# Kernel tuning notes

Hardware: AMD Instinct MI355X
Metric: run time of the kernel (lower is better)

Reference implementation:

```python
import jax, jax.numpy as jnp
import numpy as np
from jax import lax

C = 256          # fpn_feats_dim
NC = 20          # num_classes
GROUPS = 16      # GroupNorm groups
EPS = 1e-5       # GroupNorm eps (torch default)
BATCH = 8
LEVELS = [(100, 128), (50, 64), (25, 32)]  # FPN level H,W for 800x1024 image, strides 8/16/32
PRIOR_BIAS = -float(np.log((1 - 0.01) / 0.01))  # ~-4.5951, FCOS prior init


def _conv3(x, w, b):
    # 3x3 stride-1 pad-1 conv, NCHW / OIHW
    y = lax.conv_general_dilated(x, w, (1, 1), 'SAME',
                                 dimension_numbers=('NCHW', 'OIHW', 'NCHW'))
    return y + b[None, :, None, None]


def _gn(x, g, b):
    n, c, h, w = x.shape
    xr = x.reshape(n, GROUPS, c // GROUPS, h, w)
    m = xr.mean(axis=(2, 3, 4), keepdims=True)
    v = xr.var(axis=(2, 3, 4), keepdims=True)
    xr = (xr - m) * lax.rsqrt(v + EPS)
    x = xr.reshape(n, c, h, w)
    return x * g[None, :, None, None] + b[None, :, None, None]


def _forward(feat0, feat1, feat2,
             cls_conv_w, cls_conv_b, cls_gn_g, cls_gn_b, cls_out_w, cls_out_b,
             reg_conv_w, reg_conv_b, reg_gn_g, reg_gn_b,
             reg_out_w, reg_out_b, ctr_w, ctr_b):
    feats = [feat0, feat1, feat2]
    all_cls, all_reg, all_ctr = [], [], []
    for f in feats:
        n = f.shape[0]
        x = f
        for i in range(2):
            x = jax.nn.relu(_gn(_conv3(x, cls_conv_w[i], cls_conv_b[i]),
                                cls_gn_g[i], cls_gn_b[i]))
        logits = _conv3(x, cls_out_w, cls_out_b)           # [N, NC, H, W]
        # view(N,-1,NC,H,W).permute(0,3,4,1,2).reshape(N,-1,NC) == NHWC flatten
        all_cls.append(logits.transpose(0, 2, 3, 1).reshape(n, -1, NC))
        t = f
        for i in range(2):
            t = jax.nn.relu(_gn(_conv3(t, reg_conv_w[i], reg_conv_b[i]),
                                reg_gn_g[i], reg_gn_b[i]))
        # bbox_reg = Sequential(conv, ReLU), then an extra relu in forward (idempotent)
        bbox = jax.nn.relu(jax.nn.relu(_conv3(t, reg_out_w, reg_out_b)))  # [N,4,H,W]
        all_reg.append(bbox.transpose(0, 2, 3, 1).reshape(n, -1, 1))      # [N,H*W*4,1]
        ctr = _conv3(t, ctr_w, ctr_b)                                     # [N,1,H,W]
        all_ctr.append(ctr.transpose(0, 2, 3, 1).reshape(n, -1, 1))       # [N,H*W,1]
    cls_cat = jnp.concatenate(all_cls, axis=1)
    reg_cat = jnp.concatenate(all_reg, axis=1)
    ctr_cat = jnp.concatenate(all_ctr, axis=1)
    return cls_cat, reg_cat, ctr_cat


def setup_inputs() -> dict:
    key = jax.random.key(0)
    ks = jax.random.split(key, 20)
    std = 0.01
    d = {}
    for i, (h, w) in enumerate(LEVELS):
        d[f"feat{i}"] = jax.random.normal(ks[i], (BATCH, C, h, w), jnp.float32)
    # classification head params
    d["cls_conv_w"] = jax.random.normal(ks[3], (2, C, C, 3, 3), jnp.float32) * std
    d["cls_conv_b"] = jnp.zeros((2, C), jnp.float32)
    d["cls_gn_g"] = jnp.ones((2, C), jnp.float32)
    d["cls_gn_b"] = jnp.zeros((2, C), jnp.float32)
    d["cls_out_w"] = jax.random.normal(ks[4], (NC, C, 3, 3), jnp.float32) * std
    d["cls_out_b"] = jnp.full((NC,), PRIOR_BIAS, jnp.float32)
    d["reg_conv_w"] = jax.random.normal(ks[5], (2, C, C, 3, 3), jnp.float32) * std
    d["reg_conv_b"] = jnp.zeros((2, C), jnp.float32)
    d["reg_gn_g"] = jnp.ones((2, C), jnp.float32)
    d["reg_gn_b"] = jnp.zeros((2, C), jnp.float32)
    d["reg_out_w"] = jax.random.normal(ks[6], (4, C, 3, 3), jnp.float32) * std
    d["reg_out_b"] = jnp.zeros((4,), jnp.float32)
    d["ctr_w"] = jax.random.normal(ks[7], (1, C, 3, 3), jnp.float32) * std
    d["ctr_b"] = jnp.zeros((1,), jnp.float32)
    return d


def reference(feat0, feat1, feat2,
              cls_conv_w, cls_conv_b, cls_gn_g, cls_gn_b, cls_out_w, cls_out_b,
              reg_conv_w, reg_conv_b, reg_gn_g, reg_gn_b,
              reg_out_w, reg_out_b, ctr_w, ctr_b):
    return _forward(feat0, feat1, feat2,
                    cls_conv_w, cls_conv_b, cls_gn_g, cls_gn_b, cls_out_w, cls_out_b,
                    reg_conv_w, reg_conv_b, reg_gn_g, reg_gn_b,
                    reg_out_w, reg_out_b, ctr_w, ctr_b)
```

## Files before the change

kernel.cpp:

```cpp
#include <hip/hip_runtime.h>

typedef unsigned short u16;
typedef __attribute__((ext_vector_type(8))) unsigned short ushort8v;
typedef __attribute__((ext_vector_type(8))) short short8v;
typedef __attribute__((ext_vector_type(4))) float floatx4;

__device__ __forceinline__ float bf2f(u16 u) {
    unsigned v = ((unsigned)u) << 16;
    float f;
    __builtin_memcpy(&f, &v, 4);
    return f;
}
__device__ __forceinline__ u16 f2bf(float f) {
    unsigned v;
    __builtin_memcpy(&v, &f, 4);
    unsigned r = (v + 0x7fffu + ((v >> 16) & 1u)) >> 16;
    return (u16)r;
}
__device__ __forceinline__ float ld(const void* p, long i, int isf) {
    return isf ? ((const float*)p)[i] : bf2f(((const u16*)p)[i]);
}
__device__ __forceinline__ void gll16(const void* g, void* l) {
    __builtin_amdgcn_global_load_lds(
        (const __attribute__((address_space(1))) unsigned int*)g,
        (__attribute__((address_space(3))) unsigned int*)l, 16, 0, 0);
}

__global__ void detect_dtype(const u16* __restrict__ gng, int* __restrict__ flag) {
    if (threadIdx.x == 0) flag[0] = (gng[0] == 0x3F80u) ? 0 : 1;
}

__global__ void conv_params(const void* ccb, const void* cgg, const void* cgb,
                            const void* rcb, const void* rgg, const void* rgb,
                            const void* cob, const void* rob, const void* ctb,
                            const int* __restrict__ flag, u16* __restrict__ dst) {
    const int isf = flag[0];
    for (int i = threadIdx.x; i < 3104; i += 256) {
        const void* src; int off;
        if (i < 512)       { src = ccb; off = i; }
        else if (i < 1024) { src = cgg; off = i - 512; }
        else if (i < 1536) { src = cgb; off = i - 1024; }
        else if (i < 2048) { src = rcb; off = i - 1536; }
        else if (i < 2560) { src = rgg; off = i - 2048; }
        else if (i < 3072) { src = rgb; off = i - 2560; }
        else if (i < 3092) { src = cob; off = i - 3072; }
        else if (i < 3096) { src = rob; off = i - 3092; }
        else if (i < 3097) { src = ctb; off = 0; }
        else               { dst[i] = 0; continue; }
        dst[i] = f2bf(ld(src, off, isf));
    }
}

__global__ void prep_w(const void* __restrict__ src, long srcOff,
                       const int* __restrict__ flag, u16* __restrict__ dst,
                       int CoutSrc, int BNr) {
    const int isf = flag[0];
    unsigned e = blockIdx.x * 256 + threadIdx.x;
    unsigned c = e & 31u;
    unsigned r = (e >> 5) % (unsigned)BNr;
    unsigned kc = (e / (32u * BNr)) % 72u;
    unsigned nt = e / (32u * BNr * 72u);
    unsigned co = nt * BNr + r;
    unsigned tap = kc >> 3, ci = (kc & 7u) * 32u + c;
    u16 v = 0;
    if (co < (unsigned)CoutSrc)
        v = f2bf(ld(src, srcOff + (long)(co * 256u + ci) * 9 + tap, isf));
    dst[e] = v;
}

__global__ void prep_w_regctr(const void* __restrict__ wreg, const void* __restrict__ wctr,
                              const int* __restrict__ flag, u16* __restrict__ dst) {
    const int isf = flag[0];
    unsigned e = blockIdx.x * 256 + threadIdx.x;
    unsigned c = e & 31u;
    unsigned r = (e >> 5) & 31u;
    unsigned kc = e / 1024u;
    unsigned tap = kc >> 3, ci = (kc & 7u) * 32u + c;
    u16 v = 0;
    if (r < 4u)       v = f2bf(ld(wreg, (long)(r * 256u + ci) * 9 + tap, isf));
    else if (r == 4u) v = f2bf(ld(wctr, (long)ci * 9 + tap, isf));
    dst[e] = v;
}

__global__ void zero_border(u16* __restrict__ buf, int H, int Wp, int Hp, int NB) {
    const int nb = 2 * Wp + 2 * H;
    unsigned idx = blockIdx.x * 256 + threadIdx.x;
    unsigned ch = idx & 31u;
    unsigned rem = idx >> 5;
    unsigned n = rem / (unsigned)nb;
    unsigned b = rem - n * nb;
    if (n >= (unsigned)NB) return;
    int ppos;
    if ((int)b < Wp) ppos = (int)b;
    else if ((int)b < 2 * Wp) ppos = (Hp - 1) * Wp + ((int)b - Wp);
    else {
        int r = (int)b - 2 * Wp;
        ppos = (1 + (r >> 1)) * Wp + ((r & 1) ? (Wp - 1) : 0);
    }
    ushort8v z = {};
    *(ushort8v*)(buf + ((long)n * (Hp * Wp) + ppos) * 256 + ch * 8) = z;
}

__global__ void nchw_to_nhwc_pad(const void* __restrict__ src, long srcOff,
                                 const int* __restrict__ flag, u16* __restrict__ dst,
                                 int S, int W, int Wp, int HpWp) {
    const int isf = flag[0];
    __shared__ u16 t[64][34];
    const int tid = threadIdx.x;
    const int n = blockIdx.z, ct = blockIdx.y;
    const int s0 = blockIdx.x * 32;
    const long base = srcOff + ((long)(n * 256 + ct * 64)) * S + s0;
#pragma unroll
    for (int i = 0; i < 8; ++i) {
        int c = i * 8 + (tid >> 5);
        t[c][tid & 31] = f2bf(ld(src, base + (long)c * S + (tid & 31), isf));
    }
    __syncthreads();
#pragma unroll
    for (int i = 0; i < 8; ++i) {
        int px = i * 4 + (tid >> 6);
        int s = s0 + px;
        int y = s / W, x = s - y * W;
        dst[((long)n * HpWp + (long)(y + 1) * Wp + (x + 1)) * 256 + ct * 64 + (tid & 63)] =
            t[tid & 63][px];
    }
}

__global__ void gn_stats(const u16* __restrict__ x, float* __restrict__ stats, int S) {
    const int n = blockIdx.x >> 4, g = blockIdx.x & 15;
    const int tid = threadIdx.x;
    float sum = 0.f, sq = 0.f;
    const u16* base = x + (long)n * S * 256 + g * 16 + (tid & 7) * 2;
    for (int p = tid >> 3; p < S; p += 32) {
        unsigned v = *(const unsigned*)(base + (long)p * 256);
        float x0 = bf2f((u16)(v & 0xffffu));
        float x1 = bf2f((u16)(v >> 16));
        sum += x0 + x1;
        sq += x0 * x0 + x1 * x1;
    }
#pragma unroll
    for (int off = 32; off > 0; off >>= 1) {
        sum += __shfl_down(sum, off, 64);
        sq  += __shfl_down(sq, off, 64);
    }
    __shared__ float red[8];
    const int wave = tid >> 6, lane = tid & 63;
    if (lane == 0) { red[wave * 2] = sum; red[wave * 2 + 1] = sq; }
    __syncthreads();
    if (tid == 0) {
        stats[(n * 16 + g) * 2]     = red[0] + red[2] + red[4] + red[6];
        stats[(n * 16 + g) * 2 + 1] = red[1] + red[3] + red[5] + red[7];
    }
}

__global__ void gn_norm_relu(const u16* __restrict__ x, const float* __restrict__ stats,
                             const u16* __restrict__ gam, const u16* __restrict__ bet,
                             u16* __restrict__ outp, int S, int W, int Wp, int HpWp,
                             float invC) {
    unsigned idx = blockIdx.x * 256 + threadIdx.x;
    unsigned c8 = idx & 31u;
    unsigned rem = idx >> 5;
    unsigned p = rem % (unsigned)S;
    unsigned n = rem / (unsigned)S;
    unsigned c0 = c8 * 8u;
    unsigned g = c0 >> 4;
    float sum = stats[(n * 16 + g) * 2], sq = stats[(n * 16 + g) * 2 + 1];
    float mean = sum * invC;
    float var = fmaxf(sq * invC - mean * mean, 0.f);
    float rstd = rsqrtf(var + 1e-5f);
    ushort8v v = *(const ushort8v*)(x + ((long)(n * S + p)) * 256 + c0);
    unsigned y = p / (unsigned)W, xc = p - y * W;
    u16* dst = outp + ((long)n * HpWp + (long)(y + 1) * Wp + (xc + 1)) * 256 + c0;
    ushort8v o;
#pragma unroll
    for (int j = 0; j < 8; ++j) {
        float xv = bf2f(v[j]);
        float r = (xv - mean) * rstd * bf2f(gam[c0 + j]) + bf2f(bet[c0 + j]);
        o[j] = f2bf(fmaxf(r, 0.f));
    }
    *(ushort8v*)dst = o;
}

template <int BN, int MODE>
__global__ __launch_bounds__(256, 2)
void conv_gemm(const u16* __restrict__ Ap, const u16* __restrict__ Wb,
               const u16* __restrict__ bias, const u16* __restrict__ bias2,
               void* __restrict__ outp, long ob1, long ob2,
               const int* __restrict__ dflag,
               int M, int n0, int S, int W, int Wp, int HpWp, int prefS) {
    static_assert(BN == 256 || BN == 32, "");
    constexpr int MI = (BN == 256) ? 4 : 2;
    constexpr int NI = (BN == 256) ? 8 : 2;
    constexpr int ASZ = 128 * 32;
    constexpr int BSZ = BN * 32;
    __shared__ __align__(16) u16 ldsA[3 * ASZ];
    __shared__ __align__(16) u16 ldsB[3 * BSZ];
    const int tid = threadIdx.x;
    const int lane = tid & 63, wave = tid >> 6;

    const unsigned NTg = gridDim.y;
    const unsigned nwg = gridDim.x * NTg;
    const unsigned lin = blockIdx.y * gridDim.x + blockIdx.x;
    const unsigned qq = nwg >> 3, rr = nwg & 7u;
    const unsigned xcd = lin & 7u, pos = lin >> 3;
    const unsigned wg =
        (xcd < rr ? xcd * (qq + 1u) : rr * (qq + 1u) + (xcd - rr) * qq) + pos;
    const int nt = (int)(wg % NTg);
    const int m0 = (int)(wg / NTg) * 128;

    int isf = 0;
    if (MODE != 0) isf = dflag[0];

    const int csw = ((lane & 3) ^ ((lane >> 2) & 3)) * 16;

    const int r0 = 32 * wave + (lane >> 2);
    int mA0 = m0 + r0;        if (mA0 > M - 1) mA0 = M - 1;
    int mA1 = m0 + r0 + 16;   if (mA1 > M - 1) mA1 = M - 1;
    const char* aL0;
    const char* aL1;
    {
        int n8 = mA0 / S, s = mA0 - n8 * S, y = s / W, x = s - y * W;
        aL0 = (const char*)(Ap + ((long)n8 * HpWp + (long)(y + 1) * Wp + (x + 1)) * 256)
              + csw;
        n8 = mA1 / S; s = mA1 - n8 * S; y = s / W; x = s - y * W;
        aL1 = (const char*)(Ap + ((long)n8 * HpWp + (long)(y + 1) * Wp + (x + 1)) * 256)
              + csw;
    }
    u16* lA0 = ldsA + (32 * wave) * 32;
    u16* lA1 = ldsA + (32 * wave + 16) * 32;

    const u16* b_tile = Wb + (long)nt * 72 * BN * 32;
    const char* bsrc0;
    u16* lB0;
    if (BN == 256) {
        bsrc0 = (const char*)b_tile + (64 * wave + (lane >> 2)) * 64 + csw;
        lB0 = ldsB + (64 * wave) * 32;
    } else {
        bsrc0 = (const char*)b_tile + (16 * wave + (lane >> 2)) * 64 + csw;
        lB0 = ldsB + wave * 16 * 32;
    }

    auto STAGE = [&](int kc, int p) {
        const int tap = kc >> 3;
        const int ty = tap / 3;
        const int tx = tap - ty * 3;
        const long aoffB = (long)((ty - 1) * Wp + (tx - 1)) * 512 + (kc & 7) * 64;
        gll16(aL0 + aoffB, lA0 + p * ASZ);
        gll16(aL1 + aoffB, lA1 + p * ASZ);
        if (BN == 256) {
            const char* bs = bsrc0 + (long)kc * 16384;
            u16* lb = lB0 + p * BSZ;
            gll16(bs,        lb);
            gll16(bs + 1024, lb + 16 * 32);
            gll16(bs + 2048, lb + 32 * 32);
            gll16(bs + 3072, lb + 48 * 32);
        } else {
            if (wave < 2) gll16(bsrc0 + (long)kc * 2048, lB0 + p * BSZ);
        }
    };

    floatx4 acc[MI][NI] = {};

    const int wm = (BN == 256) ? (wave & 1) * 64 : wave * 32;
    const int wn = (BN == 256) ? (wave >> 1) * 128 : 0;
    const int fr = lane & 15, q = lane >> 4;
    const int qs = (q ^ (fr & 3)) * 8;
    const u16* fA = ldsA + (wm + fr) * 32 + qs;
    const u16* fB = ldsB + (wn + fr) * 32 + qs;

    STAGE(0, 0);
    STAGE(1, 1);
    STAGE(2, 2);

    int p = 0;
#pragma unroll 1
    for (int kc = 0; kc < 70; ++kc) {
        if constexpr (BN == 256)
            asm volatile("s_waitcnt vmcnt(12)" ::: "memory");
        else
            asm volatile("s_waitcnt vmcnt(4)" ::: "memory");
        __builtin_amdgcn_s_barrier();
        short8v af[MI], bf[NI];
        const u16* fAp = fA + p * ASZ;
        const u16* fBp = fB + p * BSZ;
#pragma unroll
        for (int i = 0; i < MI; ++i) af[i] = *(const short8v*)(fAp + i * 16 * 32);
#pragma unroll
        for (int j = 0; j < NI; ++j) bf[j] = *(const short8v*)(fBp + j * 16 * 32);
        asm volatile("s_waitcnt lgkmcnt(0)" ::: "memory");
        __builtin_amdgcn_s_barrier();
        if (kc < 69) STAGE(kc + 3, p);
#pragma unroll
        for (int i = 0; i < MI; ++i)
#pragma unroll
            for (int j = 0; j < NI; ++j)
                acc[i][j] = __builtin_amdgcn_mfma_f32_16x16x32_bf16(af[i], bf[j],
                                                                    acc[i][j], 0, 0, 0);
        p = (p == 2) ? 0 : p + 1;
    }
    {
        if constexpr (BN == 256)
            asm volatile("s_waitcnt vmcnt(6)" ::: "memory");
        else
            asm volatile("s_waitcnt vmcnt(2)" ::: "memory");
        __builtin_amdgcn_s_barrier();
        short8v af[MI], bf[NI];
        const u16* fAp = fA + 1 * ASZ;
        const u16* fBp = fB + 1 * BSZ;
#pragma unroll
        for (int i = 0; i < MI; ++i) af[i] = *(const short8v*)(fAp + i * 16 * 32);
#pragma unroll
        for (int j = 0; j < NI; ++j) bf[j] = *(const short8v*)(fBp + j * 16 * 32);
#pragma unroll
        for (int i = 0; i < MI; ++i)
#pragma unroll
            for (int j = 0; j < NI; ++j)
                acc[i][j] = __builtin_amdgcn_mfma_f32_16x16x32_bf16(af[i], bf[j],
                                                                    acc[i][j], 0, 0, 0);
    }
    {
        asm volatile("s_waitcnt vmcnt(0)" ::: "memory");
        __builtin_amdgcn_s_barrier();
        short8v af[MI], bf[NI];
        const u16* fAp = fA + 2 * ASZ;
        const u16* fBp = fB + 2 * BSZ;
#pragma unroll
        for (int i = 0; i < MI; ++i) af[i] = *(const short8v*)(fAp + i * 16 * 32);
#pragma unroll
        for (int j = 0; j < NI; ++j) bf[j] = *(const short8v*)(fBp + j * 16 * 32);
#pragma unroll
        for (int i = 0; i < MI; ++i)
#pragma unroll
            for (int j = 0; j < NI; ++j)
                acc[i][j] = __builtin_amdgcn_mfma_f32_16x16x32_bf16(af[i], bf[j],
                                                                    acc[i][j], 0, 0, 0);
    }

    if (MODE == 0) {
        u16* out = (u16*)outp;
#pragma unroll
        for (int j = 0; j < NI; ++j) {
            const int co = nt * BN + wn + j * 16 + fr;
            const float bv = bf2f(bias[co]);
#pragma unroll
            for (int i = 0; i < MI; ++i) {
#pragma unroll
                for (int r = 0; r < 4; ++r) {
                    const int mg = m0 + wm + i * 16 + q * 4 + r;
                    if (mg < M)
                        out[(long)mg * 256 + co] = f2bf(acc[i][j][r] + bv);
                }
            }
        }
    } else {
#pragma unroll
        for (int i = 0; i < MI; ++i) {
#pragma unroll
            for (int r = 0; r < 4; ++r) {
                const int mg = m0 + wm + i * 16 + q * 4 + r;
                if (mg >= M) continue;
                const int n8 = mg / S;
                const int s = mg - n8 * S;
                const long gi = n0 + n8;
#pragma unroll
                for (int j = 0; j < NI; ++j) {
                    const int co = wn + j * 16 + fr;
                    const float v = acc[i][j][r];
                    long oi = -1;
                    float val = 0.f;
                    if (MODE == 1) {
                        if (co < 20) {
                            oi = ob1 + gi * 336000 + (long)(prefS + s) * 20 + co;
                            val = v + bf2f(bias[co]);
                        }
                    } else {
                        if (co < 4) {
                            oi = ob1 + gi * 67200 + (long)(prefS + s) * 4 + co;
                            val = fmaxf(v + bf2f(bias[co]), 0.f);
                        } else if (co == 4) {
                            oi = ob2 + gi * 16800 + (prefS + s);
                            val = v + bf2f(bias2[0]);
                        }
                    }
                    if (oi >= 0) {
                        if (isf) ((float*)outp)[oi] = val;
                        else     ((u16*)outp)[oi] = f2bf(val);
                    }
                }
            }
        }
    }
}

extern "C" void kernel_launch(void* const* d_in, const int* in_sizes, int n_in,
                              void* d_out, int out_size, void* d_ws, size_t ws_size,
                              hipStream_t stream) {
    (void)in_sizes; (void)n_in; (void)out_size;
    const void* feat[3]   = {d_in[0], d_in[1], d_in[2]};
    const void* cls_conv_w = d_in[3];
    const void* cls_conv_b = d_in[4];
    const void* cls_gn_g   = d_in[5];
    const void* cls_gn_b   = d_in[6];
    const void* cls_out_w  = d_in[7];
    const void* cls_out_b  = d_in[8];
    const void* reg_conv_w = d_in[9];
    const void* reg_conv_b = d_in[10];
    const void* reg_gn_g   = d_in[11];
    const void* reg_gn_b   = d_in[12];
    const void* reg_out_w  = d_in[13];
    const void* reg_out_b  = d_in[14];
    const void* ctr_w      = d_in[15];
    const void* ctr_b      = d_in[16];

    char* ws = (char*)d_ws;
    int*  flag     = (int*)ws;
    u16*  params   = (u16*)(ws + 1024);
    u16*  Wb       = (u16*)(ws + 8192);
    float* stats   = (float*)(ws + 5021696);
    const size_t base = 5022720;
    const size_t per_img = 6789120ull + 6553600ull + 6789120ull;
    int NB = 8;
    while (NB > 1 && base + (size_t)NB * per_img > ws_size) NB >>= 1;
    u16* feat_pad  = (u16*)(ws + base);
    u16* conv_out  = (u16*)(ws + base + (size_t)NB * 6789120ull);
    u16* norm_pad  = (u16*)(ws + base + (size_t)NB * (6789120ull + 6553600ull));

    detect_dtype<<<1, 64, 0, stream>>>((const u16*)cls_gn_g, flag);
    conv_params<<<1, 256, 0, stream>>>(cls_conv_b, cls_gn_g, cls_gn_b,
                                       reg_conv_b, reg_gn_g, reg_gn_b,
                                       cls_out_b, reg_out_b, ctr_b, flag, params);
    prep_w<<<2304, 256, 0, stream>>>(cls_conv_w, 0,      flag, Wb + 0,       256, 256);
    prep_w<<<2304, 256, 0, stream>>>(cls_conv_w, 589824, flag, Wb + 589824,  256, 256);
    prep_w<<<2304, 256, 0, stream>>>(reg_conv_w, 0,      flag, Wb + 1179648, 256, 256);
    prep_w<<<2304, 256, 0, stream>>>(reg_conv_w, 589824, flag, Wb + 1769472, 256, 256);
    prep_w<<<288,  256, 0, stream>>>(cls_out_w,  0,      flag, Wb + 2359296, 20, 32);
    prep_w_regctr<<<288, 256, 0, stream>>>(reg_out_w, ctr_w, flag, Wb + 2433024);

    const int Hs[3] = {100, 50, 25}, Wss[3] = {128, 64, 32};
    const int prefSs[3] = {0, 12800, 16000};

    for (int l = 0; l < 3; ++l) {
        const int H = Hs[l], W = Wss[l], S = H * W;
        const int Hp = H + 2, Wp = W + 2, HpWp = Hp * Wp;
        const int prefS = prefSs[l];
        const int nb = 2 * Wp + 2 * H;
        const float invC = 1.0f / (16.0f * (float)S);

        for (int n0 = 0; n0 < 8; n0 += NB) {
            const int M = NB * S;
            const int mtiles = (M + 127) / 128;
            const int zb_blocks = (NB * nb * 32 + 255) / 256;

            zero_border<<<zb_blocks, 256, 0, stream>>>(feat_pad, H, Wp, Hp, NB);
            zero_border<<<zb_blocks, 256, 0, stream>>>(norm_pad, H, Wp, Hp, NB);
            nchw_to_nhwc_pad<<<dim3(S / 32, 4, NB), 256, 0, stream>>>(
                feat[l], (long)n0 * 256 * S, flag, feat_pad, S, W, Wp, HpWp);

            conv_gemm<256, 0><<<dim3(mtiles, 1), 256, 0, stream>>>(
                feat_pad, Wb + 0, params + 0, nullptr, conv_out, 0, 0, flag,
                M, n0, S, W, Wp, HpWp, 0);
            gn_stats<<<NB * 16, 256, 0, stream>>>(conv_out, stats, S);
            gn_norm_relu<<<M / 8, 256, 0, stream>>>(conv_out, stats, params + 512,
                                                    params + 1024, norm_pad,
                                                    S, W, Wp, HpWp, invC);
            conv_gemm<256, 0><<<dim3(mtiles, 1), 256, 0, stream>>>(
                norm_pad, Wb + 589824, params + 256, nullptr, conv_out, 0, 0, flag,
                M, n0, S, W, Wp, HpWp, 0);
            gn_stats<<<NB * 16, 256, 0, stream>>>(conv_out, stats, S);
            gn_norm_relu<<<M / 8, 256, 0, stream>>>(conv_out, stats, params + 512 + 256,
                                                    params + 1024 + 256, norm_pad,
                                                    S, W, Wp, HpWp, invC);
            conv_gemm<32, 1><<<dim3(mtiles, 1), 256, 0, stream>>>(
                norm_pad, Wb + 2359296, params + 3072, nullptr, d_out, 0, 0, flag,
                M, n0, S, W, Wp, HpWp, prefS);

            conv_gemm<256, 0><<<dim3(mtiles, 1), 256, 0, stream>>>(
                feat_pad, Wb + 1179648, params + 1536, nullptr, conv_out, 0, 0, flag,
                M, n0, S, W, Wp, HpWp, 0);
            gn_stats<<<NB * 16, 256, 0, stream>>>(conv_out, stats, S);
            gn_norm_relu<<<M / 8, 256, 0, stream>>>(conv_out, stats, params + 2048,
                                                    params + 2560, norm_pad,
                                                    S, W, Wp, HpWp, invC);
            conv_gemm<256, 0><<<dim3(mtiles, 1), 256, 0, stream>>>(
                norm_pad, Wb + 1769472, params + 1536 + 256, nullptr, conv_out, 0, 0, flag,
                M, n0, S, W, Wp, HpWp, 0);
            gn_stats<<<NB * 16, 256, 0, stream>>>(conv_out, stats, S);
            gn_norm_relu<<<M / 8, 256, 0, stream>>>(conv_out, stats, params + 2048 + 256,
                                                    params + 2560 + 256, norm_pad,
                                                    S, W, Wp, HpWp, invC);
            conv_gemm<32, 2><<<dim3(mtiles, 1), 256, 0, stream>>>(
                norm_pad, Wb + 2433024, params + 3092, params + 3096,
                d_out, 2688000, 3225600, flag,
                M, n0, S, W, Wp, HpWp, prefS);
        }
    }
}
```

Before: 2.315 ms.

## Restructure triple-buffered GEMM loop to one barrier per step with MFMA priority

The K loop of the conv GEMM is reorganised. It now keeps two stages in flight and issues the next prefetch into the buffer freed in the previous iteration, so each step needs one barrier instead of two. Per-wave vmcnt waits now match the number of loads each wave issued. MFMA blocks are wrapped in s_setprio so compute waves get scheduling priority. The cost is a shorter prefetch distance, which could expose global-load latency, and the wait counts must stay exactly right for the result to be correct.

```diff
diff --git a/kernel.cpp b/kernel.cpp
--- a/kernel.cpp
+++ b/kernel.cpp
@@ -268,18 +268,7 @@
     const u16* fA = ldsA + (wm + fr) * 32 + qs;
     const u16* fB = ldsB + (wn + fr) * 32 + qs;
 
-    STAGE(0, 0);
-    STAGE(1, 1);
-    STAGE(2, 2);
-
-    int p = 0;
-#pragma unroll 1
-    for (int kc = 0; kc < 70; ++kc) {
-        if constexpr (BN == 256)
-            asm volatile("s_waitcnt vmcnt(12)" ::: "memory");
-        else
-            asm volatile("s_waitcnt vmcnt(4)" ::: "memory");
-        __builtin_amdgcn_s_barrier();
+    auto COMPUTE = [&](int p) {
         short8v af[MI], bf[NI];
         const u16* fAp = fA + p * ASZ;
         const u16* fBp = fB + p * BSZ;
@@ -287,53 +276,49 @@
         for (int i = 0; i < MI; ++i) af[i] = *(const short8v*)(fAp + i * 16 * 32);
 #pragma unroll
         for (int j = 0; j < NI; ++j) bf[j] = *(const short8v*)(fBp + j * 16 * 32);
-        asm volatile("s_waitcnt lgkmcnt(0)" ::: "memory");
-        __builtin_amdgcn_s_barrier();
-        if (kc < 69) STAGE(kc + 3, p);
+        __builtin_amdgcn_s_setprio(1);
 #pragma unroll
         for (int i = 0; i < MI; ++i)
 #pragma unroll
             for (int j = 0; j < NI; ++j)
                 acc[i][j] = __builtin_amdgcn_mfma_f32_16x16x32_bf16(af[i], bf[j],
                                                                     acc[i][j], 0, 0, 0);
+        __builtin_amdgcn_s_setprio(0);
+    };
+
+    STAGE(0, 0);
+    STAGE(1, 1);
+
+    int p = 0;
+    int pn = 2;
+#pragma unroll 1
+    for (int kc = 0; kc < 70; ++kc) {
+        if constexpr (BN == 256) {
+            asm volatile("s_waitcnt vmcnt(6)" ::: "memory");
+        } else {
+            if (wave < 2) asm volatile("s_waitcnt vmcnt(3)" ::: "memory");
+            else          asm volatile("s_waitcnt vmcnt(2)" ::: "memory");
+        }
+        __builtin_amdgcn_s_barrier();
+        STAGE(kc + 2, pn);
+        COMPUTE(p);
+        pn = p;
         p = (p == 2) ? 0 : p + 1;
     }
     {
-        if constexpr (BN == 256)
+        if constexpr (BN == 256) {
             asm volatile("s_waitcnt vmcnt(6)" ::: "memory");
-        else
-            asm volatile("s_waitcnt vmcnt(2)" ::: "memory");
+        } else {
+            if (wave < 2) asm volatile("s_waitcnt vmcnt(3)" ::: "memory");
+            else          asm volatile("s_waitcnt vmcnt(2)" ::: "memory");
+        }
         __builtin_amdgcn_s_barrier();
-        short8v af[MI], bf[NI];
-        const u16* fAp = fA + 1 * ASZ;
-        const u16* fBp = fB + 1 * BSZ;
-#pragma unroll
-        for (int i = 0; i < MI; ++i) af[i] = *(const short8v*)(fAp + i * 16 * 32);
-#pragma unroll
-        for (int j = 0; j < NI; ++j) bf[j] = *(const short8v*)(fBp + j * 16 * 32);
-#pragma unroll
-        for (int i = 0; i < MI; ++i)
-#pragma unroll
-            for (int j = 0; j < NI; ++j)
-                acc[i][j] = __builtin_amdgcn_mfma_f32_16x16x32_bf16(af[i], bf[j],
-                                                                    acc[i][j], 0, 0, 0);
+        COMPUTE(1);
     }
     {
         asm volatile("s_waitcnt vmcnt(0)" ::: "memory");
         __builtin_amdgcn_s_barrier();
-        short8v af[MI], bf[NI];
-        const u16* fAp = fA + 2 * ASZ;
-        const u16* fBp = fB + 2 * BSZ;
-#pragma unroll
-        for (int i = 0; i < MI; ++i) af[i] = *(const short8v*)(fAp + i * 16 * 32);
-#pragma unroll
-        for (int j = 0; j < NI; ++j) bf[j] = *(const short8v*)(fBp + j * 16 * 32);
-#pragma unroll
-        for (int i = 0; i < MI; ++i)
-#pragma unroll
-            for (int j = 0; j < NI; ++j)
-                acc[i][j] = __builtin_amdgcn_mfma_f32_16x16x32_bf16(af[i], bf[j],
-                                                                    acc[i][j], 0, 0, 0);
+        COMPUTE(2);
     }
 
     if (MODE == 0) {
```

New measurement: 2.600 ms. +12.3%, slower.

## Load B weight fragments directly from global into registers, bypassing LDS

Applied to the files above, without the earlier changes.

For the BN=256 conv GEMM path, weight (B) fragments are now loaded straight from global memory into registers with inline global_load_dwordx4, double-buffered across two register sets, instead of being staged through LDS. Only the A (activation) tile still goes through LDS with a 3-slot ring, and prefetch distance drops from 3 to 2. This cuts LDS traffic and LDS footprint, which may allow higher occupancy. In exchange it uses more VGPRs for the two B buffers and relies on hand-set vmcnt counts and L2 hits for the weight reads.

```diff
diff --git a/kernel.cpp b/kernel.cpp
--- a/kernel.cpp
+++ b/kernel.cpp
@@ -192,9 +192,9 @@
     constexpr int MI = (BN == 256) ? 4 : 2;
     constexpr int NI = (BN == 256) ? 8 : 2;
     constexpr int ASZ = 128 * 32;
-    constexpr int BSZ = BN * 32;
+    constexpr int BSZ = 32 * 32;
     __shared__ __align__(16) u16 ldsA[3 * ASZ];
-    __shared__ __align__(16) u16 ldsB[3 * BSZ];
+    __shared__ __align__(16) u16 ldsB[(BN == 32) ? 3 * BSZ : 4];
     const int tid = threadIdx.x;
     const int lane = tid & 63, wave = tid >> 6;
 
@@ -229,111 +229,125 @@
     u16* lA0 = ldsA + (32 * wave) * 32;
     u16* lA1 = ldsA + (32 * wave + 16) * 32;
 
-    const u16* b_tile = Wb + (long)nt * 72 * BN * 32;
-    const char* bsrc0;
-    u16* lB0;
-    if (BN == 256) {
-        bsrc0 = (const char*)b_tile + (64 * wave + (lane >> 2)) * 64 + csw;
-        lB0 = ldsB + (64 * wave) * 32;
-    } else {
-        bsrc0 = (const char*)b_tile + (16 * wave + (lane >> 2)) * 64 + csw;
-        lB0 = ldsB + wave * 16 * 32;
-    }
-
-    auto STAGE = [&](int kc, int p) {
-        const int tap = kc >> 3;
-        const int ty = tap / 3;
-        const int tx = tap - ty * 3;
-        const long aoffB = (long)((ty - 1) * Wp + (tx - 1)) * 512 + (kc & 7) * 64;
-        gll16(aL0 + aoffB, lA0 + p * ASZ);
-        gll16(aL1 + aoffB, lA1 + p * ASZ);
-        if (BN == 256) {
-            const char* bs = bsrc0 + (long)kc * 16384;
-            u16* lb = lB0 + p * BSZ;
-            gll16(bs,        lb);
-            gll16(bs + 1024, lb + 16 * 32);
-            gll16(bs + 2048, lb + 32 * 32);
-            gll16(bs + 3072, lb + 48 * 32);
-        } else {
-            if (wave < 2) gll16(bsrc0 + (long)kc * 2048, lB0 + p * BSZ);
-        }
-    };
-
-    floatx4 acc[MI][NI] = {};
-
     const int wm = (BN == 256) ? (wave & 1) * 64 : wave * 32;
     const int wn = (BN == 256) ? (wave >> 1) * 128 : 0;
     const int fr = lane & 15, q = lane >> 4;
     const int qs = (q ^ (fr & 3)) * 8;
     const u16* fA = ldsA + (wm + fr) * 32 + qs;
-    const u16* fB = ldsB + (wn + fr) * 32 + qs;
-
-    STAGE(0, 0);
-    STAGE(1, 1);
-    STAGE(2, 2);
-
-    int p = 0;
+
+    floatx4 acc[MI][NI] = {};
+    const u16* b_tile = Wb + (long)nt * 72 * BN * 32;
+
+    if constexpr (BN == 256) {
+        auto STAGE = [&](int kc, int p) {
+            const int tap = kc >> 3;
+            const int ty = tap / 3;
+            const int tx = tap - ty * 3;
+            const long aoffB = (long)((ty - 1) * Wp + (tx - 1)) * 512 + (kc & 7) * 64;
+            gll16(aL0 + aoffB, lA0 + p * ASZ);
+            gll16(aL1 + aoffB, lA1 + p * ASZ);
+        };
+        const char* bgbase = (const char*)b_tile + (wn + fr) * 64 + q * 16;
+        auto BLOAD = [&](int kc, short8v (&bf)[NI]) {
+            const char* ba = bgbase + (long)kc * 16384;
+#pragma unroll
+            for (int j = 0; j < NI; ++j)
+                asm volatile("global_load_dwordx4 %0, %1, off"
+                             : "=&v"(bf[j]) : "v"(ba + j * 1024) : "memory");
+        };
+
+        short8v bfA[NI], bfB[NI];
+        int p = 0, pn = 2;
+
+        auto ITER = [&](int kc, short8v (&bfc)[NI], bool last, bool issue) {
+            if (last) asm volatile("s_waitcnt vmcnt(0)" ::: "memory");
+            else      asm volatile("s_waitcnt vmcnt(10)" ::: "memory");
+            __builtin_amdgcn_sched_barrier(0);
+            __builtin_amdgcn_s_barrier();
+            short8v af[MI];
+            const u16* fAp = fA + p * ASZ;
+#pragma unroll
+            for (int i = 0; i < MI; ++i) af[i] = *(const short8v*)(fAp + i * 16 * 32);
+            asm volatile("s_waitcnt lgkmcnt(0)" ::: "memory");
+            __builtin_amdgcn_s_barrier();
+#pragma unroll
+            for (int i = 0; i < MI; ++i)
+#pragma unroll
+                for (int j = 0; j < NI; ++j)
+                    acc[i][j] = __builtin_amdgcn_mfma_f32_16x16x32_bf16(
+                        af[i], bfc[j], acc[i][j], 0, 0, 0);
+            if (issue) {
+                BLOAD(kc + 2, bfc);
+                STAGE(kc + 2, pn);
+            }
+            pn = p;
+            p = (p == 2) ? 0 : p + 1;
+        };
+
+        BLOAD(0, bfA); STAGE(0, 0);
+        BLOAD(1, bfB); STAGE(1, 1);
 #pragma unroll 1
-    for (int kc = 0; kc < 70; ++kc) {
-        if constexpr (BN == 256)
-            asm volatile("s_waitcnt vmcnt(12)" ::: "memory");
-        else
+        for (int kc2 = 0; kc2 < 70; kc2 += 2) {
+            ITER(kc2,     bfA, false, true);
+            ITER(kc2 + 1, bfB, false, true);
+        }
+        ITER(70, bfA, false, false);
+        ITER(71, bfB, true,  false);
+    } else {
+        const char* bsrc0 = (const char*)b_tile + (16 * wave + (lane >> 2)) * 64 + csw;
+        u16* lB0 = ldsB + wave * 16 * 32;
+        auto STAGE = [&](int kc, int p) {
+            const int tap = kc >> 3;
+            const int ty = tap / 3;
+            const int tx = tap - ty * 3;
+            const long aoffB = (long)((ty - 1) * Wp + (tx - 1)) * 512 + (kc & 7) * 64;
+            gll16(aL0 + aoffB, lA0 + p * ASZ);
+            gll16(aL1 + aoffB, lA1 + p * ASZ);
+            if (wave < 2) gll16(bsrc0 + (long)kc * 2048, lB0 + p * BSZ);
+        };
+        const u16* fB = ldsB + (wn + fr) * 32 + qs;
+        STAGE(0, 0); STAGE(1, 1); STAGE(2, 2);
+        int p = 0;
+#pragma unroll 1
+        for (int kc = 0; kc < 70; ++kc) {
             asm volatile("s_waitcnt vmcnt(4)" ::: "memory");
-        __builtin_amdgcn_s_barrier();
-        short8v af[MI], bf[NI];
-        const u16* fAp = fA + p * ASZ;
-        const u16* fBp = fB + p * BSZ;
-#pragma unroll
-        for (int i = 0; i < MI; ++i) af[i] = *(const short8v*)(fAp + i * 16 * 32);
-#pragma unroll
-        for (int j = 0; j < NI; ++j) bf[j] = *(const short8v*)(fBp + j * 16 * 32);
-        asm volatile("s_waitcnt lgkmcnt(0)" ::: "memory");
-        __builtin_amdgcn_s_barrier();
-        if (kc < 69) STAGE(kc + 3, p);
-#pragma unroll
-        for (int i = 0; i < MI; ++i)
-#pragma unroll
-            for (int j = 0; j < NI; ++j)
-                acc[i][j] = __builtin_amdgcn_mfma_f32_16x16x32_bf16(af[i], bf[j],
-                                                                    acc[i][j], 0, 0, 0);
-        p = (p == 2) ? 0 : p + 1;
-    }
-    {
-        if constexpr (BN == 256)
-            asm volatile("s_waitcnt vmcnt(6)" ::: "memory");
-        else
-            asm volatile("s_waitcnt vmcnt(2)" ::: "memory");
-        __builtin_amdgcn_s_barrier();
-        short8v af[MI], bf[NI];
-        const u16* fAp = fA + 1 * ASZ;
-        const u16* fBp = fB + 1 * BSZ;
-#pragma unroll
-        for (int i = 0; i < MI; ++i) af[i] = *(const short8v*)(fAp + i * 16 * 32);
-#pragma unroll
-        for (int j = 0; j < NI; ++j) bf[j] = *(const short8v*)(fBp + j * 16 * 32);
-#pragma unroll
-        for (int i = 0; i < MI; ++i)
-#pragma unroll
-            for (int j = 0; j < NI; ++j)
-                acc[i][j] = __builtin_amdgcn_mfma_f32_16x16x32_bf16(af[i], bf[j],
-                                                                    acc[i][j], 0, 0, 0);
-    }
-    {
-        asm volatile("s_waitcnt vmcnt(0)" ::: "memory");
-        __builtin_amdgcn_s_barrier();
-        short8v af[MI], bf[NI];
-        const u16* fAp = fA + 2 * ASZ;
-        const u16* fBp = fB + 2 * BSZ;
-#pragma unroll
-        for (int i = 0; i < MI; ++i) af[i] = *(const short8v*)(fAp + i * 16 * 32);
-#pragma unroll
-        for (int j = 0; j < NI; ++j) bf[j] = *(const short8v*)(fBp + j * 16 * 32);
-#pragma unroll
-        for (int i = 0; i < MI; ++i)
-#pragma unroll
-            for (int j = 0; j < NI; ++j)
-                acc[i][j] = __builtin_amdgcn_mfma_f32_16x16x32_bf16(af[i], bf[j],
-                                                                    acc[i][j], 0, 0, 0);
+            __builtin_amdgcn_s_barrier();
+            short8v af[MI], bf[NI];
+            const u16* fAp = fA + p * ASZ;
+            const u16* fBp = fB + p * BSZ;
+#pragma unroll
+            for (int i = 0; i < MI; ++i) af[i] = *(const short8v*)(fAp + i * 16 * 32);
+#pragma unroll
+            for (int j = 0; j < NI; ++j) bf[j] = *(const short8v*)(fBp + j * 16 * 32);
+            asm volatile("s_waitcnt lgkmcnt(0)" ::: "memory");
+            __builtin_amdgcn_s_barrier();
+            if (kc < 69) STAGE(kc + 3, p);
+#pragma unroll
+            for (int i = 0; i < MI; ++i)
+#pragma unroll
+                for (int j = 0; j < NI; ++j)
+                    acc[i][j] = __builtin_amdgcn_mfma_f32_16x16x32_bf16(
+                        af[i], bf[j], acc[i][j], 0, 0, 0);
+            p = (p == 2) ? 0 : p + 1;
+        }
+        for (int t = 0; t < 2; ++t) {
+            if (t == 0) asm volatile("s_waitcnt vmcnt(2)" ::: "memory");
+            else        asm volatile("s_waitcnt vmcnt(0)" ::: "memory");
+            __builtin_amdgcn_s_barrier();
+            short8v af[MI], bf[NI];
+            const u16* fAp = fA + (1 + t) * ASZ;
+            const u16* fBp = fB + (1 + t) * BSZ;
+#pragma unroll
+            for (int i = 0; i < MI; ++i) af[i] = *(const short8v*)(fAp + i * 16 * 32);
+#pragma unroll
+            for (int j = 0; j < NI; ++j) bf[j] = *(const short8v*)(fBp + j * 16 * 32);
+#pragma unroll
+            for (int i = 0; i < MI; ++i)
+#pragma unroll
+                for (int j = 0; j < NI; ++j)
+                    acc[i][j] = __builtin_amdgcn_mfma_f32_16x16x32_bf16(
+                        af[i], bf[j], acc[i][j], 0, 0, 0);
+        }
     }
 
     if (MODE == 0) {
```

Result: no change. 2.352 ms (+1.6%).
